# Kernel optimization log

Hardware: AMD Instinct MI355X
Metric: run time of the kernel (lower is better)

## Reference

```python
import jax, jax.numpy as jnp
import numpy as np

B, S, H = 1, 2048, 2048
QL, KVL = 1536, 512
NH, NOPE, ROPE, VD = 16, 128, 64, 128
IH, ID = 16, 128
TOPK = 512
EPS = 1e-6


def _rms_norm(x, g):
    return x * jax.lax.rsqrt(jnp.mean(x * x, -1, keepdims=True) + EPS) * g


def _layer_norm(x, g, b):
    m = jnp.mean(x, -1, keepdims=True)
    v = jnp.mean((x - m) ** 2, -1, keepdims=True)
    return (x - m) * jax.lax.rsqrt(v + EPS) * g + b


def _rope(x, cos, sin):
    # x: [B,S,h,D] (D even), cos/sin: [S,D//2]; neox-style rotate-halves
    x1, x2 = jnp.split(x, 2, -1)
    c = cos[None, :, None, :]
    s = sin[None, :, None, :]
    return jnp.concatenate([x1 * c - x2 * s, x1 * s + x2 * c], -1)


def setup_inputs() -> dict:
    key = jax.random.key(0)
    ks = jax.random.split(key, 10)
    rn = lambda k, sh: (jax.random.normal(k, sh) * 0.02).astype(jnp.float32)
    pos = jnp.arange(S, dtype=jnp.float32)
    inv = 1.0 / (10000.0 ** (jnp.arange(0, ROPE, 2, dtype=jnp.float32) / ROPE))
    ang = pos[:, None] * inv[None, :]  # [S, ROPE//2]
    return {
        "hidden_states": jax.random.normal(ks[0], (B, S, H), jnp.float32),
        "cos": jnp.cos(ang),
        "sin": jnp.sin(ang),
        "Wq_a": rn(ks[1], (H, QL)),
        "q_a_gamma": jnp.ones((QL,), jnp.float32),
        "Wq_b": rn(ks[2], (QL, NH * (NOPE + ROPE))),
        "Wkv_a": rn(ks[3], (H, KVL + ROPE)),
        "kv_a_gamma": jnp.ones((KVL,), jnp.float32),
        "Wkv_b": rn(ks[4], (KVL, NH * (NOPE + VD))),
        "Wo": rn(ks[5], (NH * VD, H)),
        "Wq_idx": rn(ks[6], (QL, IH * ID)),
        "Wk_idx": rn(ks[7], (H, ID)),
        "Ww_idx": rn(ks[8], (H, IH)),
        "kn_gamma": jnp.ones((ID,), jnp.float32),
        "kn_beta": jnp.zeros((ID,), jnp.float32),
        "topk": TOPK,
    }


def reference(hidden_states, cos, sin, Wq_a, q_a_gamma, Wq_b, Wkv_a, kv_a_gamma,
              Wkv_b, Wo, Wq_idx, Wk_idx, Ww_idx, kn_gamma, kn_beta, topk):
    b, s, _ = hidden_states.shape
    softmax_scale = (NOPE + ROPE) ** -0.5

    # ---- low-rank Q path ----
    q_a = _rms_norm(hidden_states @ Wq_a, q_a_gamma)                 # [B,S,QL]
    q = (q_a @ Wq_b).reshape(b, s, NH, NOPE + ROPE)
    q_nope, q_pe = q[..., :NOPE], _rope(q[..., NOPE:], cos, sin)

    # ---- latent KV path (MQA rope key) ----
    kv = hidden_states @ Wkv_a                                        # [B,S,KVL+ROPE]
    kv_c = _rms_norm(kv[..., :KVL], kv_a_gamma)
    k_pe = _rope(kv[..., KVL:][:, :, None, :], cos, sin)[:, :, 0]     # [B,S,ROPE]
    kvb = (kv_c @ Wkv_b).reshape(b, s, NH, NOPE + VD)
    k_nope, v = kvb[..., :NOPE], kvb[..., NOPE:]

    # ---- lightning indexer: I[t,s] = sum_h w[t,h] * relu(q_idx[t,h] . k_idx[s]) ----
    qi = (q_a @ Wq_idx).reshape(b, s, IH, ID)
    qi = jnp.concatenate([_rope(qi[..., :ROPE], cos, sin), qi[..., ROPE:]], -1)
    ki = _layer_norm(hidden_states @ Wk_idx, kn_gamma, kn_beta)       # [B,S,ID]
    ki = jnp.concatenate([_rope(ki[:, :, None, :ROPE], cos, sin)[:, :, 0], ki[..., ROPE:]], -1)
    w = hidden_states @ Ww_idx                                        # [B,S,IH]
    s_h = jax.nn.relu(jnp.einsum('bthd,bsd->bhts', qi, ki)) * (ID ** -0.5)
    idx_scores = jnp.einsum('bth,bhts->bts', w, s_h)                  # [B,S,S]

    causal = jnp.tril(jnp.ones((s, s), bool))
    idx_scores = jnp.where(causal[None], idx_scores, -jnp.inf)
    top_idx = jax.lax.top_k(idx_scores, topk)[1]                      # [B,S,topk]
    sel = jnp.zeros((b, s, s), bool).at[
        jnp.arange(b)[:, None, None], jnp.arange(s)[None, :, None], top_idx
    ].set(True)
    mask = sel & causal[None]                                         # [B,S,S]

    # ---- sparse MLA attention over selected tokens ----
    scores = (jnp.einsum('bthd,bshd->bhts', q_nope, k_nope)
              + jnp.einsum('bthd,bsd->bhts', q_pe, k_pe)) * softmax_scale
    scores = jnp.where(mask[:, None], scores, -jnp.inf)
    attn = jax.nn.softmax(scores, -1)                                 # [B,NH,S,S]
    out = jnp.einsum('bhts,bshd->bthd', attn, v).reshape(b, s, NH * VD)
    return out @ Wo                                                   # [B,S,H]
```

## Files before the change

### kernel.cpp

```cpp
#include <hip/hip_runtime.h>
#include <cstdint>
#include <cstddef>
#include <cmath>

typedef unsigned long long u64;
typedef __attribute__((ext_vector_type(8))) short bf16x8;
typedef __attribute__((ext_vector_type(4))) float f32x4;

static constexpr int S_    = 2048;
static constexpr int H_    = 2048;
static constexpr int TOPKC = 512;

#define SCALE_ATTN 0.07216878364870323f
#define ISCALE_ID  0.08838834764831845f
#define EPS_F 1e-6f

__device__ inline unsigned short f2b(float f) {
  unsigned u = __float_as_uint(f);
  return (unsigned short)((u + 0x7FFFu + ((u >> 16) & 1u)) >> 16);
}
__device__ inline float b2f(unsigned short b) {
  return __uint_as_float(((unsigned)b) << 16);
}
__device__ inline void gload16(const unsigned short* g, unsigned short* l) {
  __builtin_amdgcn_global_load_lds((const __attribute__((address_space(1))) void*)g,
                                   (__attribute__((address_space(3))) void*)l, 16, 0, 0);
}

__global__ __launch_bounds__(256) void k_gemm_bf16(
    const unsigned short* __restrict__ A, int lda,
    const unsigned short* __restrict__ Bt, int K,
    void* __restrict__ C, int ldc, int N, int out_bf16) {
  __shared__ unsigned short As[128 * 64];
  __shared__ unsigned short Bs[128 * 64];
  int nwg = gridDim.x * gridDim.y;
  int orig = blockIdx.y * gridDim.x + blockIdx.x;
  int q = nwg >> 3, r = nwg & 7;
  int xcd = orig & 7, sub = orig >> 3;
  int wgid = (xcd < r ? xcd * (q + 1) : r * (q + 1) + (xcd - r) * q) + sub;
  int by = wgid / gridDim.x, bx = wgid - by * gridDim.x;
  const int bm = by * 128, bn = bx * 128;
  const int tid = threadIdx.x;
  const int lane = tid & 63, w = tid >> 6;
  const int wm = w >> 1, wn = w & 1;
  const int l15 = lane & 15, quarter = lane >> 4;
  const int srow = (lane >> 3), scol = (lane & 7) * 8;

  f32x4 acc[4][4];
#pragma unroll
  for (int i = 0; i < 4; i++)
#pragma unroll
    for (int j = 0; j < 4; j++) acc[i][j] = (f32x4){0.f, 0.f, 0.f, 0.f};

  for (int k0 = 0; k0 < K; k0 += 64) {
    __syncthreads();
#pragma unroll
    for (int i = 0; i < 4; i++) {
      int r0 = w * 32 + i * 8;
      gload16(A  + (size_t)(bm + r0 + srow) * lda + k0 + scol, &As[r0 * 64]);
      gload16(Bt + (size_t)(bn + r0 + srow) * K   + k0 + scol, &Bs[r0 * 64]);
    }
    __syncthreads();
#pragma unroll
    for (int kc = 0; kc < 2; kc++) {
      bf16x8 af[4], bfr[4];
#pragma unroll
      for (int mf = 0; mf < 4; mf++)
        af[mf] = *(const bf16x8*)(As + (wm * 64 + mf * 16 + l15) * 64 + kc * 32 + quarter * 8);
#pragma unroll
      for (int nf = 0; nf < 4; nf++)
        bfr[nf] = *(const bf16x8*)(Bs + (wn * 64 + nf * 16 + l15) * 64 + kc * 32 + quarter * 8);
#pragma unroll
      for (int mf = 0; mf < 4; mf++)
#pragma unroll
        for (int nf = 0; nf < 4; nf++)
          acc[mf][nf] = __builtin_amdgcn_mfma_f32_16x16x32_bf16(af[mf], bfr[nf], acc[mf][nf], 0, 0, 0);
    }
  }
#pragma unroll
  for (int mf = 0; mf < 4; mf++)
#pragma unroll
    for (int nf = 0; nf < 4; nf++)
#pragma unroll
      for (int r2 = 0; r2 < 4; r2++) {
        int grow = bm + wm * 64 + mf * 16 + quarter * 4 + r2;
        int gcol = bn + wn * 64 + nf * 16 + l15;
        if (gcol < N) {
          if (out_bf16) ((unsigned short*)C)[(size_t)grow * ldc + gcol] = f2b(acc[mf][nf][r2]);
          else          ((float*)C)[(size_t)grow * ldc + gcol] = acc[mf][nf][r2];
        }
      }
}

__device__ inline void tcast_tile(const float* __restrict__ W, int K, int N,
                                  unsigned short* __restrict__ dst,
                                  int r, int ntx, int tid, float (*T)[33]) {
  int xt = r % ntx, kt = r / ntx;
  int n0 = xt * 32, k0 = kt * 32;
#pragma unroll
  for (int i = 0; i < 4; i++) {
    int idx = tid + 256 * i;
    int rr = idx >> 5, c = idx & 31;
    T[rr][c] = W[(size_t)(k0 + rr) * N + n0 + c];
  }
  __syncthreads();
#pragma unroll
  for (int i = 0; i < 4; i++) {
    int idx = tid + 256 * i;
    int rr = idx >> 5, c = idx & 31;
    dst[(size_t)(n0 + rr) * K + k0 + c] = f2b(T[c][rr]);
  }
}

__global__ __launch_bounds__(256) void k_tcast_p1(
    const float* __restrict__ Wq_a, const float* __restrict__ Wkv_a,
    const float* __restrict__ Wk_idx, const float* __restrict__ Ww_idx,
    const float* __restrict__ hs, unsigned short* __restrict__ hs_b,
    unsigned short* __restrict__ WT) {
  __shared__ float T[32][33];
  int bid = blockIdx.x, tid = threadIdx.x;
  if (bid < 3072)      tcast_tile(Wq_a,  2048, 1536, WT,                          bid,        48, tid, T);
  else if (bid < 4224) tcast_tile(Wkv_a, 2048,  576, WT + (size_t)1536 * 2048,    bid - 3072, 18, tid, T);
  else if (bid < 4480) tcast_tile(Wk_idx,2048,  128, WT + (size_t)2112 * 2048,    bid - 4224,  4, tid, T);
  else if (bid < 4608) {
    int idx = (bid - 4480) * 256 + tid;
    int k = idx >> 4, n = idx & 15;
    WT[(size_t)(2240 + n) * 2048 + k] = f2b(Ww_idx[(size_t)k * 16 + n]);
  } else {
    int idx = ((bid - 4608) * 256 + tid) * 4;
    const float* ip = hs + idx;
    unsigned short* op = hs_b + idx;
    op[0] = f2b(ip[0]); op[1] = f2b(ip[1]); op[2] = f2b(ip[2]); op[3] = f2b(ip[3]);
  }
}

__global__ __launch_bounds__(256) void k_tcast_p2(
    const float* __restrict__ Wq_b, const float* __restrict__ Wq_idx,
    unsigned short* __restrict__ WT) {
  __shared__ float T[32][33];
  int bid = blockIdx.x, tid = threadIdx.x;
  if (bid < 4608) tcast_tile(Wq_b,   1536, 3072, WT,                        bid,        96, tid, T);
  else            tcast_tile(Wq_idx, 1536, 2048, WT + (size_t)3072 * 1536,  bid - 4608, 64, tid, T);
}

__global__ __launch_bounds__(256) void k_tcast_p3(
    const float* __restrict__ Wkv_b, const float* __restrict__ Wo,
    unsigned short* __restrict__ WT) {
  __shared__ float T[32][33];
  int bid = blockIdx.x, tid = threadIdx.x;
  if (bid < 2048) tcast_tile(Wkv_b,  512, 4096, WT,                       bid,        128, tid, T);
  else            tcast_tile(Wo,    2048, 2048, WT + (size_t)4096 * 512,  bid - 2048,  64, tid, T);
}

__global__ __launch_bounds__(256) void k_norms(
    const float* __restrict__ fat, int stride,
    const float* __restrict__ qg, const float* __restrict__ kvg,
    const float* __restrict__ kng, const float* __restrict__ knb,
    const float* __restrict__ cosb, const float* __restrict__ sinb,
    unsigned short* __restrict__ qa_b, unsigned short* __restrict__ kvc_b,
    unsigned short* __restrict__ kpe_b, unsigned short* __restrict__ ki_b) {
  int t = blockIdx.x, tid = threadIdx.x;
  const float* p = fat + (size_t)t * stride;
  __shared__ float red[256];
  __shared__ float buf[128];
  float x[6]; float s = 0.f;
#pragma unroll
  for (int i = 0; i < 6; i++) { x[i] = p[tid + 256 * i]; s += x[i] * x[i]; }
  red[tid] = s; __syncthreads();
  for (int st = 128; st > 0; st >>= 1) { if (tid < st) red[tid] += red[tid + st]; __syncthreads(); }
  float scl = rsqrtf(red[0] * (1.f / 1536.f) + EPS_F);
#pragma unroll
  for (int i = 0; i < 6; i++)
    qa_b[(size_t)t * 1536 + tid + 256 * i] = f2b(x[i] * scl * qg[tid + 256 * i]);
  __syncthreads();
  float y0 = p[1536 + tid], y1 = p[1792 + tid];
  red[tid] = y0 * y0 + y1 * y1; __syncthreads();
  for (int st = 128; st > 0; st >>= 1) { if (tid < st) red[tid] += red[tid + st]; __syncthreads(); }
  float scl2 = rsqrtf(red[0] * (1.f / 512.f) + EPS_F);
  kvc_b[(size_t)t * 512 + tid]       = f2b(y0 * scl2 * kvg[tid]);
  kvc_b[(size_t)t * 512 + 256 + tid] = f2b(y1 * scl2 * kvg[256 + tid]);
  if (tid < 32) {
    float a = p[2048 + tid], b = p[2080 + tid];
    float c = cosb[t * 32 + tid], sn = sinb[t * 32 + tid];
    kpe_b[(size_t)t * 64 + tid]      = f2b(a * c - b * sn);
    kpe_b[(size_t)t * 64 + 32 + tid] = f2b(a * sn + b * c);
  }
  __syncthreads();
  float z = (tid < 128) ? p[2112 + tid] : 0.f;
  red[tid] = z; __syncthreads();
  for (int st = 128; st > 0; st >>= 1) { if (tid < st) red[tid] += red[tid + st]; __syncthreads(); }
  float mean = red[0] * (1.f / 128.f);
  __syncthreads();
  float d = (tid < 128) ? (z - mean) : 0.f;
  red[tid] = d * d; __syncthreads();
  for (int st = 128; st > 0; st >>= 1) { if (tid < st) red[tid] += red[tid + st]; __syncthreads(); }
  float var = red[0] * (1.f / 128.f);
  if (tid < 128) buf[tid] = d * rsqrtf(var + EPS_F) * kng[tid] + knb[tid];
  __syncthreads();
  if (tid < 128) {
    float outv;
    if (tid < 32) {
      float c = cosb[t * 32 + tid], sn = sinb[t * 32 + tid];
      outv = buf[tid] * c - buf[tid + 32] * sn;
    } else if (tid < 64) {
      int j = tid - 32;
      float c = cosb[t * 32 + j], sn = sinb[t * 32 + j];
      outv = buf[j] * sn + buf[tid] * c;
    } else outv = buf[tid];
    ki_b[(size_t)t * 128 + tid] = f2b(outv);
  }
}

__global__ __launch_bounds__(256) void k_rope_b(unsigned short* __restrict__ base, int rowstride, int nh,
                                                int hstride, int off, const float* __restrict__ cosb,
                                                const float* __restrict__ sinb, int total) {
  int idx = blockIdx.x * 256 + threadIdx.x;
  if (idx >= total) return;
  int i = idx & 31, h = (idx >> 5) % nh, t = idx / (32 * nh);
  unsigned short* p = base + (size_t)t * rowstride + h * hstride + off;
  float x1 = b2f(p[i]), x2 = b2f(p[i + 32]);
  float c = cosb[t * 32 + i], s = sinb[t * 32 + i];
  p[i] = f2b(x1 * c - x2 * s);
  p[i + 32] = f2b(x1 * s + x2 * c);
}

__global__ __launch_bounds__(256) void k_idx_mfma(
    const unsigned short* __restrict__ qi_b, int qpitch,
    const unsigned short* __restrict__ ki_b,
    const float* __restrict__ wb, int wstride,
    float* __restrict__ out) {
  int bid = blockIdx.x;
  int tb = (int)((sqrtf(8.f * bid + 1.f) - 1.f) * 0.5f);
  while ((tb + 1) * (tb + 2) / 2 <= bid) tb++;
  while (tb * (tb + 1) / 2 > bid) tb--;
  int sb = bid - tb * (tb + 1) / 2;
  int t0 = tb * 64, s0 = sb * 64;

  int tid = threadIdx.x, lane = tid & 63, w = tid >> 6;
  int wm = w >> 1, wn = w & 1;
  int l15 = lane & 15, quarter = lane >> 4;

  __shared__ unsigned short Ks[64 * 128];
  __shared__ unsigned short Qs[2][64 * 128];
  __shared__ float Ws[64][16];

  int srow_[4], scc_[4];
#pragma unroll
  for (int i = 0; i < 4; i++) {
    int row = w * 16 + i * 4 + (lane >> 4);
    srow_[i] = row;
    scc_[i] = (lane & 15) ^ (row & 7);
  }
#pragma unroll
  for (int i = 0; i < 4; i++) {
    gload16(ki_b + (size_t)(s0 + srow_[i]) * 128 + scc_[i] * 8, &Ks[(w * 16 + i * 4) * 128]);
    gload16(qi_b + (size_t)(t0 + srow_[i]) * qpitch + scc_[i] * 8, &Qs[0][(w * 16 + i * 4) * 128]);
  }
  for (int i = tid; i < 64 * 16; i += 256) Ws[i >> 4][i & 15] = wb[(size_t)(t0 + (i >> 4)) * wstride + (i & 15)];
  __syncthreads();

  bf16x8 bfr[2][4];
#pragma unroll
  for (int nf = 0; nf < 2; nf++) {
    int row = wn * 32 + nf * 16 + l15;
    int rx = (row & 7) << 3;
#pragma unroll
    for (int kc = 0; kc < 4; kc++)
      bfr[nf][kc] = *(const bf16x8*)(Ks + row * 128 + ((kc * 32 + quarter * 8) ^ rx));
  }

  f32x4 acc[2][2];
#pragma unroll
  for (int mf = 0; mf < 2; mf++)
#pragma unroll
    for (int nf = 0; nf < 2; nf++) acc[mf][nf] = (f32x4){0.f, 0.f, 0.f, 0.f};

  for (int h = 0; h < 16; h++) {
    int cur = h & 1;
    if (h < 15) {
#pragma unroll
      for (int i = 0; i < 4; i++)
        gload16(qi_b + (size_t)(t0 + srow_[i]) * qpitch + (h + 1) * 128 + scc_[i] * 8,
                &Qs[cur ^ 1][(w * 16 + i * 4) * 128]);
    }
    f32x4 acch[2][2];
#pragma unroll
    for (int mf = 0; mf < 2; mf++)
#pragma unroll
      for (int nf = 0; nf < 2; nf++) acch[mf][nf] = (f32x4){0.f, 0.f, 0.f, 0.f};

    __builtin_amdgcn_s_setprio(1);
#pragma unroll
    for (int mf = 0; mf < 2; mf++) {
      int row = wm * 32 + mf * 16 + l15;
      int rx = (row & 7) << 3;
      bf16x8 af[4];
#pragma unroll
      for (int kc = 0; kc < 4; kc++)
        af[kc] = *(const bf16x8*)(Qs[cur] + row * 128 + ((kc * 32 + quarter * 8) ^ rx));
#pragma unroll
      for (int nf = 0; nf < 2; nf++)
#pragma unroll
        for (int kc = 0; kc < 4; kc++)
          acch[mf][nf] = __builtin_amdgcn_mfma_f32_16x16x32_bf16(af[kc], bfr[nf][kc], acch[mf][nf], 0, 0, 0);
    }
    __builtin_amdgcn_s_setprio(0);
#pragma unroll
    for (int mf = 0; mf < 2; mf++) {
#pragma unroll
      for (int r = 0; r < 4; r++) {
        float wv = Ws[wm * 32 + mf * 16 + quarter * 4 + r][h];
#pragma unroll
        for (int nf = 0; nf < 2; nf++)
          acc[mf][nf][r] = fmaf(wv, fmaxf(acch[mf][nf][r], 0.f), acc[mf][nf][r]);
      }
    }
    __syncthreads();
  }
#pragma unroll
  for (int mf = 0; mf < 2; mf++)
#pragma unroll
    for (int nf = 0; nf < 2; nf++)
#pragma unroll
      for (int r = 0; r < 4; r++) {
        int t = t0 + wm * 32 + mf * 16 + quarter * 4 + r;
        int s = s0 + wn * 32 + nf * 16 + l15;
        out[(size_t)t * 2048 + s] = acc[mf][nf][r] * ISCALE_ID;
      }
}

__global__ __launch_bounds__(256) void k_topk_mask(const float* __restrict__ idx_sc, u64* __restrict__ maskw) {
  int t = blockIdx.x;
  int tid = threadIdx.x;
  int n = t + 1;
  if (n <= TOPKC) {
    if (tid < 32) {
      int lo = tid * 64, hi = lo + 63;
      u64 wv;
      if (t >= hi) wv = ~0ULL;
      else if (t < lo) wv = 0ULL;
      else wv = (~0ULL) >> (63 - (t - lo));
      maskw[(size_t)t * 32 + tid] = wv;
    }
    return;
  }
  __shared__ unsigned int u[2048];
  __shared__ int hist[256];
  __shared__ int scan[256];
  __shared__ u64 mw[32];
  __shared__ int sel_b, new_target, tie_base;
  __shared__ int wcnt[4];
  if (tid < 32) mw[tid] = 0ULL;
  const float* row = idx_sc + (size_t)t * 2048;
  for (int s = tid; s < n; s += 256) {
    unsigned int bb = __float_as_uint(row[s]);
    u[s] = (bb & 0x80000000u) ? ~bb : (bb | 0x80000000u);
  }
  __syncthreads();
  unsigned int prefix = 0;
  int target = TOPKC;
  for (int shift = 24; shift >= 0; shift -= 8) {
    hist[tid] = 0;
    __syncthreads();
    unsigned int himask = (shift == 24) ? 0u : (0xFFFFFFFFu << (shift + 8));
    for (int s = tid; s < n; s += 256) {
      unsigned int uv = u[s];
      if ((uv & himask) == prefix) atomicAdd(&hist[(uv >> shift) & 0xFF], 1);
    }
    __syncthreads();
    scan[tid] = hist[tid];
    __syncthreads();
#pragma unroll
    for (int st = 1; st < 256; st <<= 1) {
      int add = (tid + st < 256) ? scan[tid + st] : 0;
      __syncthreads();
      scan[tid] += add;
      __syncthreads();
    }
    int snext = (tid == 255) ? 0 : scan[tid + 1];
    if (scan[tid] >= target && snext < target) { sel_b = tid; new_target = target - snext; }
    __syncthreads();
    prefix |= ((unsigned int)sel_b) << shift;
    target = new_target;
    __syncthreads();
  }
  if (tid == 0) tie_base = 0;
  __syncthreads();
  int wid = tid >> 6, lane = tid & 63;
  for (int s0 = 0; s0 < n; s0 += 256) {
    int s = s0 + tid;
    bool in = (s < n);
    unsigned int uv = in ? u[s] : 0u;
    bool gt = in && (uv > prefix);
    bool tie = in && (uv == prefix);
    u64 bal = __ballot(tie);
    if (lane == 0) wcnt[wid] = __popcll(bal);
    __syncthreads();
    int wbase = tie_base;
    for (int wI = 0; wI < wid; wI++) wbase += wcnt[wI];
    int rank = wbase + __popcll(bal & ((1ULL << lane) - 1ULL));
    bool sel = gt || (tie && rank < target);
    if (sel) atomicOr(&mw[s >> 6], 1ULL << (s & 63));
    __syncthreads();
    if (tid == 0) tie_base += wcnt[0] + wcnt[1] + wcnt[2] + wcnt[3];
    __syncthreads();
  }
  if (tid < 32) maskw[(size_t)t * 32 + tid] = mw[tid];
}

__global__ __launch_bounds__(256) void k_attn_mfma(
    const unsigned short* __restrict__ qb, int qpitch,
    const unsigned short* __restrict__ kvb_b,
    const unsigned short* __restrict__ kpe_b,
    const float* __restrict__ cosb, const float* __restrict__ sinb,
    const u64* __restrict__ maskw,
    unsigned short* __restrict__ attn_b) {
  int ybm = blockIdx.x;
  int h = blockIdx.y;
  int yb = (h < 8) ? ybm : (31 - ybm);
  int t0 = yb * 64;
  int tid = threadIdx.x;
  int lane = tid & 63, wq = tid >> 6;
  int quarter = lane >> 4, l15 = lane & 15;

  __shared__ unsigned short Kd[2][64 * 192];
  __shared__ unsigned short Vts[128 * 64];

  const unsigned short* kb_base[6];
  int kb_step[6];
#pragma unroll
  for (int i = 0; i < 6; i++) {
    int slot = (wq * 6 + i) * 1024 + lane * 16;
    int rowk = slot / 384;
    int coff = slot - rowk * 384;
    int cc = (coff ^ ((rowk & 7) << 4)) >> 4;
    if (cc < 16) { kb_base[i] = kvb_b + (size_t)rowk * 4096 + h * 256 + cc * 8; kb_step[i] = 4096; }
    else         { kb_base[i] = kpe_b + (size_t)rowk * 64 + (cc - 16) * 8;      kb_step[i] = 64; }
  }
  const int vdg = tid & 15, vsp = tid >> 4;
  const unsigned short* vbase = kvb_b + (size_t)(vsp * 4) * 4096 + h * 256 + 128 + vdg * 8;

  bf16x8 qf[6];
  {
    int t = t0 + wq * 16 + l15;
    const unsigned short* qp = qb + (size_t)t * qpitch + h * 192 + quarter * 8;
#pragma unroll
    for (int kc = 0; kc < 6; kc++) qf[kc] = *(const bf16x8*)(qp + kc * 32);
    const float* cp = cosb + t * 32 + quarter * 8;
    const float* sp = sinb + t * 32 + quarter * 8;
    float4 ca = *(const float4*)cp,  cb2 = *(const float4*)(cp + 4);
    float4 sa = *(const float4*)sp,  sb2 = *(const float4*)(sp + 4);
    float carr[8] = {ca.x, ca.y, ca.z, ca.w, cb2.x, cb2.y, cb2.z, cb2.w};
    float sarr[8] = {sa.x, sa.y, sa.z, sa.w, sb2.x, sb2.y, sb2.z, sb2.w};
#pragma unroll
    for (int j = 0; j < 8; j++) {
      float x1 = b2f((unsigned short)qf[4][j]);
      float x2 = b2f((unsigned short)qf[5][j]);
      qf[4][j] = (short)f2b(x1 * carr[j] - x2 * sarr[j]);
      qf[5][j] = (short)f2b(x1 * sarr[j] + x2 * carr[j]);
    }
  }

  f32x4 o[8];
#pragma unroll
  for (int df = 0; df < 8; df++) o[df] = (f32x4){0.f, 0.f, 0.f, 0.f};
  float mcol = -__builtin_inff(), lcol = 0.f;
  const u64* mrow = maskw + (size_t)(t0 + wq * 16 + l15) * 32;
  int nsb = yb + 1;

#pragma unroll
  for (int i = 0; i < 6; i++) gload16(kb_base[i], &Kd[0][(wq * 6 + i) * 512]);
  bf16x8 vr0 = *(const bf16x8*)(vbase);
  bf16x8 vr1 = *(const bf16x8*)(vbase + 4096);
  bf16x8 vr2 = *(const bf16x8*)(vbase + 8192);
  bf16x8 vr3 = *(const bf16x8*)(vbase + 12288);
  __syncthreads();
#pragma unroll
  for (int j = 0; j < 8; j++) {
    int d = vdg * 8 + j;
    uint2 w2;
    w2.x = (unsigned)(unsigned short)vr0[j] | (((unsigned)(unsigned short)vr1[j]) << 16);
    w2.y = (unsigned)(unsigned short)vr2[j] | (((unsigned)(unsigned short)vr3[j]) << 16);
    *(uint2*)((char*)Vts + d * 128 + ((vsp * 8) ^ (((d >> 2) & 7) << 4))) = w2;
  }

  for (int sb = 0; sb < nsb; sb++) {
    int cur = sb & 1;
    __syncthreads();
    bool pf = (sb + 1 < nsb);
    if (pf) {
      size_t sn = (size_t)(sb + 1) * 64;
#pragma unroll
      for (int i = 0; i < 6; i++)
        gload16(kb_base[i] + sn * kb_step[i], &Kd[cur ^ 1][(wq * 6 + i) * 512]);
      const unsigned short* vp = vbase + sn * 4096;
      vr0 = *(const bf16x8*)(vp);
      vr1 = *(const bf16x8*)(vp + 4096);
      vr2 = *(const bf16x8*)(vp + 8192);
      vr3 = *(const bf16x8*)(vp + 12288);
    }
    const unsigned short* Kc = Kd[cur];
    f32x4 sfT[4];
#pragma unroll
    for (int sc = 0; sc < 4; sc++) {
      f32x4 a = (f32x4){0.f, 0.f, 0.f, 0.f};
      int row = sc * 16 + l15;
      int rx = (row & 7) << 4;
#pragma unroll
      for (int kc = 0; kc < 6; kc++) {
        int byte = row * 384 + ((kc * 64 + quarter * 16) ^ rx);
        bf16x8 kf = *(const bf16x8*)((const char*)Kc + byte);
        a = __builtin_amdgcn_mfma_f32_16x16x32_bf16(kf, qf[kc], a, 0, 0, 0);
      }
      sfT[sc] = a;
    }
    u64 w64 = mrow[sb];
    float p[4][4];
#pragma unroll
    for (int sc = 0; sc < 4; sc++)
#pragma unroll
      for (int r = 0; r < 4; r++) {
        int sbit = sc * 16 + quarter * 4 + r;
        bool sel = (w64 >> sbit) & 1ULL;
        p[sc][r] = sel ? sfT[sc][r] * SCALE_ATTN : -__builtin_inff();
      }
    float v = p[0][0];
#pragma unroll
    for (int sc = 0; sc < 4; sc++)
#pragma unroll
      for (int r = 0; r < 4; r++) v = fmaxf(v, p[sc][r]);
    v = fmaxf(v, __shfl_xor(v, 16));
    v = fmaxf(v, __shfl_xor(v, 32));
    float mn = fmaxf(mcol, v);
    bool dead = (mn == -__builtin_inff());
    float scl = dead ? 1.f : __expf(mcol - mn);
#pragma unroll
    for (int sc = 0; sc < 4; sc++)
#pragma unroll
      for (int r = 0; r < 4; r++)
        p[sc][r] = dead ? 0.f : __expf(p[sc][r] - mn);
    mcol = dead ? mcol : mn;
    float rs = 0.f;
#pragma unroll
    for (int sc = 0; sc < 4; sc++)
#pragma unroll
      for (int r = 0; r < 4; r++) rs += p[sc][r];
    rs += __shfl_xor(rs, 16);
    rs += __shfl_xor(rs, 32);
    lcol = lcol * scl + rs;

    unsigned pk[4][2];
#pragma unroll
    for (int sc = 0; sc < 4; sc++)
#pragma unroll
      for (int rr = 0; rr < 2; rr++)
        pk[sc][rr] = (unsigned)f2b(p[sc][2 * rr]) | (((unsigned)f2b(p[sc][2 * rr + 1])) << 16);
    bf16x8 pa[2];
#pragma unroll
    for (int kc = 0; kc < 2; kc++) {
      union { unsigned d[4]; bf16x8 v; } pu;
#pragma unroll
      for (int jj = 0; jj < 4; jj++) {
        int src = ((quarter & 1) * 2 + (jj >> 1)) * 16 + l15;
        unsigned lo = (unsigned)__shfl((int)pk[kc * 2][jj & 1], src);
        unsigned hi = (unsigned)__shfl((int)pk[kc * 2 + 1][jj & 1], src);
        pu.d[jj] = (quarter < 2) ? lo : hi;
      }
      pa[kc] = pu.v;
    }
    float sclr[4];
#pragma unroll
    for (int r = 0; r < 4; r++) sclr[r] = __shfl(scl, quarter * 4 + r);
#pragma unroll
    for (int df = 0; df < 8; df++)
#pragma unroll
      for (int r = 0; r < 4; r++) o[df][r] *= sclr[r];
#pragma unroll
    for (int kc = 0; kc < 2; kc++)
#pragma unroll
      for (int df = 0; df < 8; df++) {
        int d = df * 16 + l15;
        int vbyte = d * 128 + ((kc * 64 + quarter * 16) ^ (((d >> 2) & 7) << 4));
        bf16x8 vf = *(const bf16x8*)((const char*)Vts + vbyte);
        o[df] = __builtin_amdgcn_mfma_f32_16x16x32_bf16(pa[kc], vf, o[df], 0, 0, 0);
      }
    __syncthreads();
    if (pf) {
#pragma unroll
      for (int j = 0; j < 8; j++) {
        int d = vdg * 8 + j;
        uint2 w2;
        w2.x = (unsigned)(unsigned short)vr0[j] | (((unsigned)(unsigned short)vr1[j]) << 16);
        w2.y = (unsigned)(unsigned short)vr2[j] | (((unsigned)(unsigned short)vr3[j]) << 16);
        *(uint2*)((char*)Vts + d * 128 + ((vsp * 8) ^ (((d >> 2) & 7) << 4))) = w2;
      }
    }
  }
  float inv = (lcol > 0.f) ? 1.f / lcol : 0.f;
  float invr[4];
#pragma unroll
  for (int r = 0; r < 4; r++) invr[r] = __shfl(inv, quarter * 4 + r);
#pragma unroll
  for (int r = 0; r < 4; r++) {
    int t = t0 + wq * 16 + quarter * 4 + r;
    unsigned short* op = attn_b + (size_t)t * 2048 + h * 128 + l15;
#pragma unroll
    for (int df = 0; df < 8; df++) op[df * 16] = f2b(o[df][r] * invr[r]);
  }
}

extern "C" void kernel_launch(void* const* d_in, const int* in_sizes, int n_in,
                              void* d_out, int out_size, void* d_ws, size_t ws_size,
                              hipStream_t stream) {
  const float* hs     = (const float*)d_in[0];
  const float* cosb   = (const float*)d_in[1];
  const float* sinb   = (const float*)d_in[2];
  const float* Wq_a   = (const float*)d_in[3];
  const float* q_a_g  = (const float*)d_in[4];
  const float* Wq_b   = (const float*)d_in[5];
  const float* Wkv_a  = (const float*)d_in[6];
  const float* kv_a_g = (const float*)d_in[7];
  const float* Wkv_b  = (const float*)d_in[8];
  const float* Wo     = (const float*)d_in[9];
  const float* Wq_idx = (const float*)d_in[10];
  const float* Wk_idx = (const float*)d_in[11];
  const float* Ww_idx = (const float*)d_in[12];
  const float* kn_g   = (const float*)d_in[13];
  const float* kn_b   = (const float*)d_in[14];
  float* out = (float*)d_out;

  char* base = (char*)d_ws;
  size_t off = 0;
  auto alloc = [&](size_t bytes) { void* p = base + off; off += (bytes + 255) & ~size_t(255); return p; };

  float* fat1 = (float*)alloc((size_t)S_ * 2304 * 4);
  unsigned short* attn_b = (unsigned short*)fat1;
  float* idxs = (float*)alloc((size_t)S_ * 2048 * 4);
  unsigned short* fat2 = (unsigned short*)alloc((size_t)S_ * 5120 * 2);
  u64*   maskw = (u64*)alloc((size_t)S_ * 32 * 8);
  unsigned short* hs_b  = (unsigned short*)alloc((size_t)S_ * 2048 * 2);
  unsigned short* qa_b  = (unsigned short*)alloc((size_t)S_ * 1536 * 2);
  unsigned short* kvc_b = (unsigned short*)alloc((size_t)S_ * 512 * 2);
  unsigned short* kpe_b = (unsigned short*)alloc((size_t)S_ * 64 * 2);
  unsigned short* kvb_b = (unsigned short*)alloc((size_t)S_ * 4096 * 2);
  unsigned short* ki_b  = (unsigned short*)alloc((size_t)S_ * 128 * 2);
  unsigned short* WT    = (unsigned short*)alloc((size_t)5120 * 1536 * 2);

  dim3 blk(256);

  k_tcast_p1<<<dim3(8704), blk, 0, stream>>>(Wq_a, Wkv_a, Wk_idx, Ww_idx, hs, hs_b, WT);
  k_gemm_bf16<<<dim3(18, 16), blk, 0, stream>>>(hs_b, 2048, WT, 2048, fat1, 2304, 2256, 0);
  k_norms<<<dim3(S_), blk, 0, stream>>>(fat1, 2304, q_a_g, kv_a_g, kn_g, kn_b, cosb, sinb,
                                        qa_b, kvc_b, kpe_b, ki_b);
  k_tcast_p2<<<dim3(7680), blk, 0, stream>>>(Wq_b, Wq_idx, WT);
  k_gemm_bf16<<<dim3(40, 16), blk, 0, stream>>>(qa_b, 1536, WT, 1536, fat2, 5120, 5120, 1);
  k_rope_b<<<dim3((S_ * 16 * 32) / 256), blk, 0, stream>>>(fat2 + 3072, 5120, 16, 128, 0, cosb, sinb, S_ * 16 * 32);
  k_tcast_p3<<<dim3(6144), blk, 0, stream>>>(Wkv_b, Wo, WT);
  k_gemm_bf16<<<dim3(32, 16), blk, 0, stream>>>(kvc_b, 512, WT, 512, kvb_b, 4096, 4096, 1);
  k_idx_mfma<<<dim3(528), blk, 0, stream>>>(fat2 + 3072, 5120, ki_b, fat1 + 2240, 2304, idxs);
  k_topk_mask<<<dim3(S_), blk, 0, stream>>>(idxs, maskw);
  k_attn_mfma<<<dim3(32, 16), blk, 0, stream>>>(fat2, 5120, kvb_b, kpe_b, cosb, sinb, maskw, attn_b);
  k_gemm_bf16<<<dim3(16, 16), blk, 0, stream>>>(attn_b, 2048, WT + (size_t)4096 * 512, 2048, out, 2048, 2048, 0);

  (void)in_sizes; (void)n_in; (void)out_size; (void)ws_size;
}
```

Before: 351.7 us.

## Split attention key range across two blocks and merge partial softmax results

The attention kernel now launches twice as many blocks, each covering half of the causal key blocks for a query tile. Each block writes unnormalized partial outputs along with its running max and sum, and a new merge kernel combines the two halves. K/V staging drops from a double buffer to a single buffer, with the next-tile prefetch issued after the score phase. This is meant to improve occupancy and load balance on a small grid, at the cost of an extra kernel launch, extra global traffic, and bf16 rounding of the partial outputs.

```diff
diff --git a/kernel.cpp b/kernel.cpp
--- a/kernel.cpp
+++ b/kernel.cpp
@@ -414,16 +414,20 @@
     const unsigned short* __restrict__ kpe_b,
     const float* __restrict__ cosb, const float* __restrict__ sinb,
     const u64* __restrict__ maskw,
-    unsigned short* __restrict__ attn_b) {
-  int ybm = blockIdx.x;
-  int h = blockIdx.y;
-  int yb = (h < 8) ? ybm : (31 - ybm);
+    unsigned short* __restrict__ opart,
+    float* __restrict__ mlbuf) {
+  int b = blockIdx.x, h = blockIdx.y;
+  int yb0 = b >> 1, half = b & 1;
+  int yb = (h < 8) ? yb0 : (31 - yb0);
+  int n = yb + 1, h1 = (n + 1) >> 1;
+  int k0 = half ? h1 : 0;
+  int k1 = half ? n : h1;
   int t0 = yb * 64;
   int tid = threadIdx.x;
   int lane = tid & 63, wq = tid >> 6;
   int quarter = lane >> 4, l15 = lane & 15;
 
-  __shared__ unsigned short Kd[2][64 * 192];
+  __shared__ unsigned short Kd[64 * 192];
   __shared__ unsigned short Vts[128 * 64];
 
   const unsigned short* kb_base[6];
@@ -466,40 +470,28 @@
   for (int df = 0; df < 8; df++) o[df] = (f32x4){0.f, 0.f, 0.f, 0.f};
   float mcol = -__builtin_inff(), lcol = 0.f;
   const u64* mrow = maskw + (size_t)(t0 + wq * 16 + l15) * 32;
-  int nsb = yb + 1;
-
-#pragma unroll
-  for (int i = 0; i < 6; i++) gload16(kb_base[i], &Kd[0][(wq * 6 + i) * 512]);
-  bf16x8 vr0 = *(const bf16x8*)(vbase);
-  bf16x8 vr1 = *(const bf16x8*)(vbase + 4096);
-  bf16x8 vr2 = *(const bf16x8*)(vbase + 8192);
-  bf16x8 vr3 = *(const bf16x8*)(vbase + 12288);
-  __syncthreads();
-#pragma unroll
-  for (int j = 0; j < 8; j++) {
-    int d = vdg * 8 + j;
-    uint2 w2;
-    w2.x = (unsigned)(unsigned short)vr0[j] | (((unsigned)(unsigned short)vr1[j]) << 16);
-    w2.y = (unsigned)(unsigned short)vr2[j] | (((unsigned)(unsigned short)vr3[j]) << 16);
-    *(uint2*)((char*)Vts + d * 128 + ((vsp * 8) ^ (((d >> 2) & 7) << 4))) = w2;
-  }
-
-  for (int sb = 0; sb < nsb; sb++) {
-    int cur = sb & 1;
-    __syncthreads();
-    bool pf = (sb + 1 < nsb);
-    if (pf) {
-      size_t sn = (size_t)(sb + 1) * 64;
-#pragma unroll
-      for (int i = 0; i < 6; i++)
-        gload16(kb_base[i] + sn * kb_step[i], &Kd[cur ^ 1][(wq * 6 + i) * 512]);
-      const unsigned short* vp = vbase + sn * 4096;
-      vr0 = *(const bf16x8*)(vp);
-      vr1 = *(const bf16x8*)(vp + 4096);
-      vr2 = *(const bf16x8*)(vp + 8192);
-      vr3 = *(const bf16x8*)(vp + 12288);
-    }
-    const unsigned short* Kc = Kd[cur];
+
+  {
+    size_t sr = (size_t)k0 * 64;
+#pragma unroll
+    for (int i = 0; i < 6; i++) gload16(kb_base[i] + sr * kb_step[i], &Kd[(wq * 6 + i) * 512]);
+    bf16x8 v0 = *(const bf16x8*)(vbase + sr * 4096);
+    bf16x8 v1 = *(const bf16x8*)(vbase + (sr + 1) * 4096);
+    bf16x8 v2 = *(const bf16x8*)(vbase + (sr + 2) * 4096);
+    bf16x8 v3 = *(const bf16x8*)(vbase + (sr + 3) * 4096);
+    __syncthreads();
+#pragma unroll
+    for (int j = 0; j < 8; j++) {
+      int d = vdg * 8 + j;
+      uint2 w2;
+      w2.x = (unsigned)(unsigned short)v0[j] | (((unsigned)(unsigned short)v1[j]) << 16);
+      w2.y = (unsigned)(unsigned short)v2[j] | (((unsigned)(unsigned short)v3[j]) << 16);
+      *(uint2*)((char*)Vts + d * 128 + ((vsp * 8) ^ (((d >> 2) & 7) << 4))) = w2;
+    }
+  }
+
+  bf16x8 vr0, vr1, vr2, vr3;
+  for (int k = k0; k < k1; k++) {
     f32x4 sfT[4];
 #pragma unroll
     for (int sc = 0; sc < 4; sc++) {
@@ -509,12 +501,12 @@
 #pragma unroll
       for (int kc = 0; kc < 6; kc++) {
         int byte = row * 384 + ((kc * 64 + quarter * 16) ^ rx);
-        bf16x8 kf = *(const bf16x8*)((const char*)Kc + byte);
+        bf16x8 kf = *(const bf16x8*)((const char*)Kd + byte);
         a = __builtin_amdgcn_mfma_f32_16x16x32_bf16(kf, qf[kc], a, 0, 0, 0);
       }
       sfT[sc] = a;
     }
-    u64 w64 = mrow[sb];
+    u64 w64 = mrow[k];
     float p[4][4];
 #pragma unroll
     for (int sc = 0; sc < 4; sc++)
@@ -549,6 +541,19 @@
     rs += __shfl_xor(rs, 32);
     lcol = lcol * scl + rs;
 
+    __syncthreads();
+    bool pf = (k + 1 < k1);
+    if (pf) {
+      size_t sn = (size_t)(k + 1) * 64;
+#pragma unroll
+      for (int i = 0; i < 6; i++)
+        gload16(kb_base[i] + sn * kb_step[i], &Kd[(wq * 6 + i) * 512]);
+      const unsigned short* vp = vbase + sn * 4096;
+      vr0 = *(const bf16x8*)(vp);
+      vr1 = *(const bf16x8*)(vp + 4096);
+      vr2 = *(const bf16x8*)(vp + 8192);
+      vr3 = *(const bf16x8*)(vp + 12288);
+    }
     unsigned pk[4][2];
 #pragma unroll
     for (int sc = 0; sc < 4; sc++)
@@ -596,17 +601,45 @@
       }
     }
   }
-  float inv = (lcol > 0.f) ? 1.f / lcol : 0.f;
-  float invr[4];
-#pragma unroll
-  for (int r = 0; r < 4; r++) invr[r] = __shfl(inv, quarter * 4 + r);
+  unsigned short* ob = opart + (size_t)half * S_ * 2048;
 #pragma unroll
   for (int r = 0; r < 4; r++) {
     int t = t0 + wq * 16 + quarter * 4 + r;
-    unsigned short* op = attn_b + (size_t)t * 2048 + h * 128 + l15;
-#pragma unroll
-    for (int df = 0; df < 8; df++) op[df * 16] = f2b(o[df][r] * invr[r]);
-  }
+    unsigned short* op = ob + (size_t)t * 2048 + h * 128 + l15;
+#pragma unroll
+    for (int df = 0; df < 8; df++) op[df * 16] = f2b(o[df][r]);
+  }
+  if (quarter == 0) {
+    int t = t0 + wq * 16 + l15;
+    float* mp = mlbuf + (((size_t)half * S_ + t) * 16 + h) * 2;
+    mp[0] = mcol;
+    mp[1] = lcol;
+  }
+}
+
+__global__ __launch_bounds__(256) void k_attn_merge(
+    const unsigned short* __restrict__ opart, const float* __restrict__ mlbuf,
+    unsigned short* __restrict__ attn_b) {
+  int idx = blockIdx.x * 256 + threadIdx.x;
+  int dg = idx & 15, h = (idx >> 4) & 15, t = idx >> 8;
+  const float* ml0 = mlbuf + ((size_t)t * 16 + h) * 2;
+  const float* ml1 = ml0 + (size_t)S_ * 16 * 2;
+  float m0 = ml0[0], l0 = ml0[1];
+  float m1 = ml1[0], l1 = ml1[1];
+  float m = fmaxf(m0, m1);
+  float w0 = (m0 == -__builtin_inff()) ? 0.f : __expf(m0 - m);
+  float w1 = (m1 == -__builtin_inff()) ? 0.f : __expf(m1 - m);
+  float L = l0 * w0 + l1 * w1;
+  float inv = (L > 0.f) ? 1.f / L : 0.f;
+  const bf16x8 o0 = *(const bf16x8*)(opart + (size_t)t * 2048 + h * 128 + dg * 8);
+  const bf16x8 o1 = *(const bf16x8*)(opart + (size_t)S_ * 2048 + (size_t)t * 2048 + h * 128 + dg * 8);
+  bf16x8 r;
+#pragma unroll
+  for (int j = 0; j < 8; j++) {
+    float a = b2f((unsigned short)o0[j]) * w0 + b2f((unsigned short)o1[j]) * w1;
+    r[j] = (short)f2b(a * inv);
+  }
+  *(bf16x8*)(attn_b + (size_t)t * 2048 + h * 128 + dg * 8) = r;
 }
 
 extern "C" void kernel_launch(void* const* d_in, const int* in_sizes, int n_in,
@@ -636,7 +669,9 @@
   float* fat1 = (float*)alloc((size_t)S_ * 2304 * 4);
   unsigned short* attn_b = (unsigned short*)fat1;
   float* idxs = (float*)alloc((size_t)S_ * 2048 * 4);
+  unsigned short* opart = (unsigned short*)idxs;
   unsigned short* fat2 = (unsigned short*)alloc((size_t)S_ * 5120 * 2);
+  float* mlbuf = (float*)alloc((size_t)2 * S_ * 16 * 2 * 4);
   u64*   maskw = (u64*)alloc((size_t)S_ * 32 * 8);
   unsigned short* hs_b  = (unsigned short*)alloc((size_t)S_ * 2048 * 2);
   unsigned short* qa_b  = (unsigned short*)alloc((size_t)S_ * 1536 * 2);
@@ -659,7 +694,9 @@
   k_gemm_bf16<<<dim3(32, 16), blk, 0, stream>>>(kvc_b, 512, WT, 512, kvb_b, 4096, 4096, 1);
   k_idx_mfma<<<dim3(528), blk, 0, stream>>>(fat2 + 3072, 5120, ki_b, fat1 + 2240, 2304, idxs);
   k_topk_mask<<<dim3(S_), blk, 0, stream>>>(idxs, maskw);
-  k_attn_mfma<<<dim3(32, 16), blk, 0, stream>>>(fat2, 5120, kvb_b, kpe_b, cosb, sinb, maskw, attn_b);
+  k_attn_mfma<<<dim3(64, 16), blk, 0, stream>>>(fat2, 5120, kvb_b, kpe_b, cosb, sinb, maskw,
+                                                opart, mlbuf);
+  k_attn_merge<<<dim3((S_ * 16 * 16) / 256), blk, 0, stream>>>(opart, mlbuf, attn_b);
   k_gemm_bf16<<<dim3(16, 16), blk, 0, stream>>>(attn_b, 2048, WT + (size_t)4096 * 512, 2048, out, 2048, 2048, 0);
 
   (void)in_sizes; (void)n_in; (void)out_size; (void)ws_size;
```

After: 366.0 us. 1.04x slower.
